# Kernel optimization log

Hardware: AMD Instinct MI355X
Metric: run time of the kernel (lower is better)

The kernel has to match this reference:

```python
import jax, jax.numpy as jnp
import numpy as np

B, H = 4096, 256          # graphs, hidden_size
N, E = 500000, 1000000    # total nodes, total edges
FN, FE = 128, 64          # num_node_features, num_edge_features


def setup_inputs() -> dict:
    key = jax.random.key(0)
    k1, k2, k3, k4, k5, k6, k7 = jax.random.split(key, 7)
    graph_embedding = jax.random.normal(k1, (B, H), dtype=jnp.float32)
    batch = jnp.sort(jax.random.randint(k2, (N,), 0, B, dtype=jnp.int64))
    edge_index = jax.random.randint(k3, (2, E), 0, N, dtype=jnp.int64)
    s = 1.0 / np.sqrt(H)
    node_w = jax.random.uniform(k4, (FN, H), jnp.float32, -s, s)
    node_b = jax.random.uniform(k5, (FN,), jnp.float32, -s, s)
    edge_w = jax.random.uniform(k6, (FE, H), jnp.float32, -s, s)
    edge_b = jax.random.uniform(k7, (FE,), jnp.float32, -s, s)
    return {"graph_embedding": graph_embedding, "batch": batch,
            "edge_index": edge_index, "node_w": node_w, "node_b": node_b,
            "edge_w": edge_w, "edge_b": edge_b}


def reference(graph_embedding, batch, edge_index, node_w, node_b, edge_w, edge_b):
    # Expand graph embeddings to nodes: equivalent to per-graph repeat+cat
    # because `batch` is sorted by graph id.
    expanded_nodes = graph_embedding[batch]                # [N, H]
    x_hat = expanded_nodes @ node_w.T + node_b             # [N, FN]
    # Expand graph embeddings to edges via the source node's graph id.
    edge_batch = batch[edge_index[0]]                      # [E]
    expanded_edges = graph_embedding[edge_batch]           # [E, H]
    edge_hat = expanded_edges @ edge_w.T + edge_b          # [E, FE]
    return (x_hat, edge_hat)
```

## Files before the change

### kernel.cpp

```cpp
#include <hip/hip_runtime.h>


#define H   256
#define FN  128
#define FE  64
#define GPB 8

typedef float f4 __attribute__((ext_vector_type(4)));

__global__ __launch_bounds__(192) void proj_kernel(
    const float* __restrict__ ge,
    const float* __restrict__ node_w,
    const float* __restrict__ node_b,
    const float* __restrict__ edge_w,
    const float* __restrict__ edge_b,
    float* __restrict__ P,
    float* __restrict__ Q)
{
    __shared__ float sge[GPB * H];
    const int t  = threadIdx.x;
    const int g0 = blockIdx.x * GPB;

    const float4* ge4  = reinterpret_cast<const float4*>(ge + (size_t)g0 * H);
    float4*       sge4 = reinterpret_cast<float4*>(sge);
    for (int i = t; i < GPB * H / 4; i += 192) sge4[i] = ge4[i];
    __syncthreads();

    const float4* w4;
    float bias;
    if (t < FN) { w4 = reinterpret_cast<const float4*>(node_w + (size_t)t * H);      bias = node_b[t]; }
    else        { w4 = reinterpret_cast<const float4*>(edge_w + (size_t)(t-FN) * H); bias = edge_b[t-FN]; }

    float acc[GPB];
    #pragma unroll
    for (int g = 0; g < GPB; ++g) acc[g] = 0.f;

    #pragma unroll 4
    for (int k = 0; k < H / 4; ++k) {
        const float4 wv = w4[k];
        #pragma unroll
        for (int g = 0; g < GPB; ++g) {
            const float* s = sge + g * H + k * 4;
            acc[g] += wv.x * s[0] + wv.y * s[1] + wv.z * s[2] + wv.w * s[3];
        }
    }

    #pragma unroll
    for (int g = 0; g < GPB; ++g) {
        const float v = acc[g] + bias;
        if (t < FN) P[(size_t)(g0 + g) * FN + t]        = v;
        else        Q[(size_t)(g0 + g) * FE + (t - FN)] = v;
    }
}

__global__ __launch_bounds__(256) void scatter_fused(
    const int* __restrict__ batch,
    const int* __restrict__ src,
    const f4* __restrict__ P4,
    const f4* __restrict__ Q4,
    f4* __restrict__ xout,
    f4* __restrict__ eout,
    int n4, int e4, int halfBlocks, int Bm1, int Nm1)
{
    const int stride = halfBlocks * 256;
    if (blockIdx.x < (unsigned)halfBlocks) {
        for (int i = blockIdx.x * 256 + threadIdx.x; i < n4; i += stride) {
            const int row = i >> 5;
            const int c   = i & 31;
            const int g   = batch[row] & Bm1;
            __builtin_nontemporal_store(P4[(g << 5) + c], xout + i);
        }
    } else {
        for (int i = (blockIdx.x - halfBlocks) * 256 + threadIdx.x; i < e4; i += stride) {
            const int e = i >> 4;
            const int c = i & 15;
            int s = src[e];
            s = min(max(s, 0), Nm1);
            const int g = batch[s] & Bm1;
            __builtin_nontemporal_store(Q4[(g << 4) + c], eout + i);
        }
    }
}

extern "C" void kernel_launch(void* const* d_in, const int* in_sizes, int n_in,
                              void* d_out, int out_size, void* d_ws, size_t ws_size,
                              hipStream_t stream) {
    const float* ge     = (const float*)d_in[0];
    const int*   batch  = (const int*)  d_in[1];
    const int*   eidx   = (const int*)  d_in[2];
    const float* node_w = (const float*)d_in[3];
    const float* node_b = (const float*)d_in[4];
    const float* edge_w = (const float*)d_in[5];
    const float* edge_b = (const float*)d_in[6];

    const int B = in_sizes[0] / H;
    const int N = in_sizes[1];
    const int E = in_sizes[2] / 2;

    float* P = (float*)d_ws;
    float* Q = P + (size_t)B * FN;

    float* x_hat = (float*)d_out;
    float* e_hat = x_hat + (size_t)N * FN;

    proj_kernel<<<B / GPB, 192, 0, stream>>>(ge, node_w, node_b, edge_w, edge_b, P, Q);

    const int n4 = N * (FN / 4);
    const int e4 = E * (FE / 4);
    const int halfBlocks = 1024;
    scatter_fused<<<2 * halfBlocks, 256, 0, stream>>>(
        batch, eidx, (const f4*)P, (const f4*)Q, (f4*)x_hat, (f4*)e_hat,
        n4, e4, halfBlocks, B - 1, N - 1);
}
```

Measured before the change: 111.4 us.

## Stage per-row graph ids in shared memory and give each block contiguous node and edge ranges

```diff
diff --git a/kernel.cpp b/kernel.cpp
--- a/kernel.cpp
+++ b/kernel.cpp
@@ -5,6 +5,7 @@
 #define FN  128
 #define FE  64
 #define GPB 8
+#define CH  256
 
 typedef float f4 __attribute__((ext_vector_type(4)));
 
@@ -60,24 +61,50 @@
     const f4* __restrict__ Q4,
     f4* __restrict__ xout,
     f4* __restrict__ eout,
-    int n4, int e4, int halfBlocks, int Bm1, int Nm1)
+    int N, int E, int Bm1, int Nm1)
 {
-    const int stride = halfBlocks * 256;
-    if (blockIdx.x < (unsigned)halfBlocks) {
-        for (int i = blockIdx.x * 256 + threadIdx.x; i < n4; i += stride) {
-            const int row = i >> 5;
-            const int c   = i & 31;
-            const int g   = batch[row] & Bm1;
-            __builtin_nontemporal_store(P4[(g << 5) + c], xout + i);
+    __shared__ int sg[CH];
+    const int b  = blockIdx.x;
+    const int nb = gridDim.x;
+    const int t  = threadIdx.x;
+
+    {
+        const int r0 = (int)((long long)N * b / nb);
+        const int r1 = (int)((long long)N * (b + 1) / nb);
+        for (int c0 = r0; c0 < r1; c0 += CH) {
+            const int rows = min(CH, r1 - c0);
+            __syncthreads();
+            if (t < rows) sg[t] = batch[c0 + t] & Bm1;
+            __syncthreads();
+            const int tot = rows << 5;
+            f4* outb = xout + ((size_t)c0 << 5);
+            for (int k = t; k < tot; k += 256) {
+                const int r = k >> 5, c = k & 31;
+                const int g = sg[r];
+                __builtin_nontemporal_store(P4[(g << 5) + c], outb + k);
+            }
         }
-    } else {
-        for (int i = (blockIdx.x - halfBlocks) * 256 + threadIdx.x; i < e4; i += stride) {
-            const int e = i >> 4;
-            const int c = i & 15;
-            int s = src[e];
-            s = min(max(s, 0), Nm1);
-            const int g = batch[s] & Bm1;
-            __builtin_nontemporal_store(Q4[(g << 4) + c], eout + i);
+    }
+
+    {
+        const int e0 = (int)((long long)E * b / nb);
+        const int e1 = (int)((long long)E * (b + 1) / nb);
+        for (int c0 = e0; c0 < e1; c0 += CH) {
+            const int es = min(CH, e1 - c0);
+            __syncthreads();
+            if (t < es) {
+                int s = src[c0 + t];
+                s = min(max(s, 0), Nm1);
+                sg[t] = batch[s] & Bm1;
+            }
+            __syncthreads();
+            const int tot = es << 4;
+            f4* outb = eout + ((size_t)c0 << 4);
+            for (int k = t; k < tot; k += 256) {
+                const int e = k >> 4, c = k & 15;
+                const int g = sg[e];
+                __builtin_nontemporal_store(Q4[(g << 4) + c], outb + k);
+            }
         }
     }
 }
@@ -105,10 +132,7 @@
 
     proj_kernel<<<B / GPB, 192, 0, stream>>>(ge, node_w, node_b, edge_w, edge_b, P, Q);
 
-    const int n4 = N * (FN / 4);
-    const int e4 = E * (FE / 4);
-    const int halfBlocks = 1024;
-    scatter_fused<<<2 * halfBlocks, 256, 0, stream>>>(
+    scatter_fused<<<2048, 256, 0, stream>>>(
         batch, eidx, (const f4*)P, (const f4*)Q, (f4*)x_hat, (f4*)e_hat,
-        n4, e4, halfBlocks, B - 1, N - 1);
+        N, E, B - 1, N - 1);
 }
```

After: 127.7 us. 1.15x slower.

## Stage transposed weights in LDS, precompute edge graph ids, interleave scatter loops

Applied to the files above, without the earlier changes.

```diff
diff --git a/kernel.cpp b/kernel.cpp
--- a/kernel.cpp
+++ b/kernel.cpp
@@ -5,6 +5,7 @@
 #define FN  128
 #define FE  64
 #define GPB 8
+#define KC  64
 
 typedef float f4 __attribute__((ext_vector_type(4)));
 
@@ -18,33 +19,49 @@
     float* __restrict__ Q)
 {
     __shared__ float sge[GPB * H];
+    __shared__ float swT[KC][193];
     const int t  = threadIdx.x;
     const int g0 = blockIdx.x * GPB;
 
     const float4* ge4  = reinterpret_cast<const float4*>(ge + (size_t)g0 * H);
     float4*       sge4 = reinterpret_cast<float4*>(sge);
     for (int i = t; i < GPB * H / 4; i += 192) sge4[i] = ge4[i];
-    __syncthreads();
-
-    const float4* w4;
-    float bias;
-    if (t < FN) { w4 = reinterpret_cast<const float4*>(node_w + (size_t)t * H);      bias = node_b[t]; }
-    else        { w4 = reinterpret_cast<const float4*>(edge_w + (size_t)(t-FN) * H); bias = edge_b[t-FN]; }
 
     float acc[GPB];
     #pragma unroll
     for (int g = 0; g < GPB; ++g) acc[g] = 0.f;
 
-    #pragma unroll 4
-    for (int k = 0; k < H / 4; ++k) {
-        const float4 wv = w4[k];
+    for (int k0 = 0; k0 < H; k0 += KC) {
+        __syncthreads();
         #pragma unroll
-        for (int g = 0; g < GPB; ++g) {
-            const float* s = sge + g * H + k * 4;
-            acc[g] += wv.x * s[0] + wv.y * s[1] + wv.z * s[2] + wv.w * s[3];
+        for (int j = 0; j < 16; ++j) {
+            const int idx = t + j * 192;
+            const int f   = idx >> 4;
+            const int seg = idx & 15;
+            const float* wrow = (f < FN) ? (node_w + (size_t)f * H)
+                                         : (edge_w + (size_t)(f - FN) * H);
+            const float4 wv = *reinterpret_cast<const float4*>(wrow + k0 + seg * 4);
+            swT[seg * 4 + 0][f] = wv.x;
+            swT[seg * 4 + 1][f] = wv.y;
+            swT[seg * 4 + 2][f] = wv.z;
+            swT[seg * 4 + 3][f] = wv.w;
+        }
+        __syncthreads();
+        #pragma unroll 4
+        for (int kk = 0; kk < KC; kk += 4) {
+            const float w0 = swT[kk + 0][t];
+            const float w1 = swT[kk + 1][t];
+            const float w2 = swT[kk + 2][t];
+            const float w3 = swT[kk + 3][t];
+            #pragma unroll
+            for (int g = 0; g < GPB; ++g) {
+                const float* s = sge + g * H + k0 + kk;
+                acc[g] += w0 * s[0] + w1 * s[1] + w2 * s[2] + w3 * s[3];
+            }
         }
     }
 
+    const float bias = (t < FN) ? node_b[t] : edge_b[t - FN];
     #pragma unroll
     for (int g = 0; g < GPB; ++g) {
         const float v = acc[g] + bias;
@@ -53,31 +70,39 @@
     }
 }
 
+__global__ __launch_bounds__(256) void eg_kernel(
+    const int* __restrict__ src, const int* __restrict__ batch,
+    int* __restrict__ eg, int E, int Nm1, int Bm1)
+{
+    const int stride = gridDim.x * 256;
+    for (int i = blockIdx.x * 256 + threadIdx.x; i < E; i += stride) {
+        int s = src[i];
+        s = min(max(s, 0), Nm1);
+        eg[i] = batch[s] & Bm1;
+    }
+}
+
 __global__ __launch_bounds__(256) void scatter_fused(
     const int* __restrict__ batch,
-    const int* __restrict__ src,
+    const int* __restrict__ eg,
     const f4* __restrict__ P4,
     const f4* __restrict__ Q4,
     f4* __restrict__ xout,
     f4* __restrict__ eout,
-    int n4, int e4, int halfBlocks, int Bm1, int Nm1)
+    int n4, int e4, int Bm1)
 {
-    const int stride = halfBlocks * 256;
-    if (blockIdx.x < (unsigned)halfBlocks) {
-        for (int i = blockIdx.x * 256 + threadIdx.x; i < n4; i += stride) {
-            const int row = i >> 5;
-            const int c   = i & 31;
-            const int g   = batch[row] & Bm1;
+    const int stride = gridDim.x * blockDim.x;
+    const int maxT = max(n4, e4);
+    for (int i = blockIdx.x * blockDim.x + threadIdx.x; i < maxT; i += stride) {
+        if (i < n4) {
+            const int r = i >> 5, c = i & 31;
+            const int g = batch[r] & Bm1;
             __builtin_nontemporal_store(P4[(g << 5) + c], xout + i);
         }
-    } else {
-        for (int i = (blockIdx.x - halfBlocks) * 256 + threadIdx.x; i < e4; i += stride) {
-            const int e = i >> 4;
-            const int c = i & 15;
-            int s = src[e];
-            s = min(max(s, 0), Nm1);
-            const int g = batch[s] & Bm1;
-            __builtin_nontemporal_store(Q4[(g << 4) + c], eout + i);
+        if (i < e4) {
+            const int e = i >> 4, c2 = i & 15;
+            const int g2 = eg[e];
+            __builtin_nontemporal_store(Q4[(g2 << 4) + c2], eout + i);
         }
     }
 }
@@ -97,18 +122,19 @@
     const int N = in_sizes[1];
     const int E = in_sizes[2] / 2;
 
-    float* P = (float*)d_ws;
-    float* Q = P + (size_t)B * FN;
+    float* P  = (float*)d_ws;
+    float* Q  = P + (size_t)B * FN;
+    int*   eg = (int*)(Q + (size_t)B * FE);
 
     float* x_hat = (float*)d_out;
     float* e_hat = x_hat + (size_t)N * FN;
 
     proj_kernel<<<B / GPB, 192, 0, stream>>>(ge, node_w, node_b, edge_w, edge_b, P, Q);
+    eg_kernel<<<1024, 256, 0, stream>>>(eidx, batch, eg, E, N - 1, B - 1);
 
     const int n4 = N * (FN / 4);
     const int e4 = E * (FE / 4);
-    const int halfBlocks = 1024;
-    scatter_fused<<<2 * halfBlocks, 256, 0, stream>>>(
-        batch, eidx, (const f4*)P, (const f4*)Q, (f4*)x_hat, (f4*)e_hat,
-        n4, e4, halfBlocks, B - 1, N - 1);
+    scatter_fused<<<2048, 256, 0, stream>>>(
+        batch, eg, (const f4*)P, (const f4*)Q, (f4*)x_hat, (f4*)e_hat,
+        n4, e4, B - 1);
 }
```

After: 128.1 us. 15.0% more time.
